# Optimization experiments

Hardware: AMD Instinct MI355X
Metric: run time of the kernel (lower is better)

The kernel has to match this reference:

```python
import jax, jax.numpy as jnp
import numpy as np

N_NODES = 50000
N_EDGES = 1600000
NFEAT, NHID, NCLASS = 512, 128, 40


def setup_inputs() -> dict:
    key = jax.random.key(0)
    ks = jax.random.split(key, 10)
    x = jax.random.normal(ks[0], (N_NODES, NFEAT), dtype=jnp.float32)
    edge_src = jax.random.randint(ks[1], (N_EDGES,), 0, N_NODES, dtype=jnp.int32)
    edge_dst = jax.random.randint(ks[2], (N_EDGES,), 0, N_NODES, dtype=jnp.int32)
    edge_weight = jax.random.uniform(ks[3], (N_EDGES,), dtype=jnp.float32)
    # GraphConvolution params: gc1 (nfeat->nhid), one additional (nhid->nhid), gc2 (nhid->nclass)
    s1 = 1.0 / np.sqrt(NHID)
    s2 = 1.0 / np.sqrt(NCLASS)
    W1 = jax.random.uniform(ks[4], (NFEAT, NHID), minval=-s1, maxval=s1, dtype=jnp.float32)
    b1 = jax.random.uniform(ks[5], (NHID,), minval=-s1, maxval=s1, dtype=jnp.float32)
    Wh = jax.random.uniform(ks[6], (NHID, NHID), minval=-s1, maxval=s1, dtype=jnp.float32)
    bh = jax.random.uniform(ks[7], (NHID,), minval=-s1, maxval=s1, dtype=jnp.float32)
    W2 = jax.random.uniform(ks[8], (NHID, NCLASS), minval=-s2, maxval=s2, dtype=jnp.float32)
    b2 = jax.random.uniform(ks[9], (NCLASS,), minval=-s2, maxval=s2, dtype=jnp.float32)
    return {"x": x, "edge_src": edge_src, "edge_dst": edge_dst, "edge_weight": edge_weight,
            "W1": W1, "b1": b1, "Wh": Wh, "bh": bh, "W2": W2, "b2": b2}


def reference(x, edge_src, edge_dst, edge_weight, W1, b1, Wh, bh, W2, b2):
    def spmm(h):
        # out[i] = sum_j adj[i, j] * h[j]  with adj given as weighted edge list (src=j, dst=i)
        return jax.ops.segment_sum(edge_weight[:, None] * h[edge_src], edge_dst,
                                   num_segments=x.shape[0])

    def gconv(h, W, b):
        return spmm(h @ W) + b  # dense transform then sparse aggregation

    h = jax.nn.relu(gconv(x, W1, b1))       # gc1
    h = jax.nn.relu(gconv(h, Wh, bh))        # additional hidden layer
    h = gconv(h, W2, b2)                     # gc2
    return jax.nn.log_softmax(h, axis=1)
```

## Files before the change

kernel.cpp:

```cpp
#include <hip/hip_runtime.h>
#include <hip/hip_bf16.h>
#include <math.h>

#define N_NODES 50000
#define N_EDGES 1600000
#define NFEAT 512
#define NHID 128
#define NCLASS 40

#define NBUCKETS 196
#define BUCKET_CAP 16384

typedef __attribute__((ext_vector_type(8))) short bf16x8;
typedef __attribute__((ext_vector_type(4))) float f32x4;

static __device__ __forceinline__ float asfloat_u32(unsigned int u) {
    union { unsigned int u; float f; } c;
    c.u = u;
    return c.f;
}
static __device__ __forceinline__ unsigned int asu32_f(float f) {
    union { float f; unsigned int u; } c;
    c.f = f;
    return c.u;
}
static __device__ __forceinline__ unsigned short f2bf(float f) {
    union { float f; unsigned int u; } c;
    c.f = f;
    unsigned int r = c.u + 0x7FFFu + ((c.u >> 16) & 1u);
    return (unsigned short)(r >> 16);
}

__global__ __launch_bounds__(256) void prep_kernel(const float* __restrict__ W1,
                                                   unsigned short* __restrict__ Wt1,
                                                   const float* __restrict__ Wh,
                                                   unsigned short* __restrict__ Wth,
                                                   int* __restrict__ bucketCursor) {
    int idx = blockIdx.x * 256 + threadIdx.x;
    if (idx < NFEAT * NHID) {
        int k = idx >> 7;
        int n = idx & 127;
        Wt1[(size_t)n * NFEAT + k] = f2bf(W1[idx]);
    } else if (idx < NFEAT * NHID + NHID * NHID) {
        int j = idx - NFEAT * NHID;
        int k = j >> 7;
        int n = j & 127;
        Wth[(size_t)n * NHID + k] = f2bf(Wh[j]);
    } else {
        int j = idx - (NFEAT * NHID + NHID * NHID);
        if (j < NBUCKETS) bucketCursor[j] = j * BUCKET_CAP;
    }
}

#define LDP 40
#define GEMM_LDS_BYTES ((64 + 128) * LDP * 2)

template <bool A_IS_BF16>
static __device__ __forceinline__ void gemm64_body(const void* __restrict__ Ap,
                                                   const unsigned short* __restrict__ Wt,
                                                   unsigned short* __restrict__ C,
                                                   const int M, const int K,
                                                   char* smem, int bid) {
    unsigned short* As = (unsigned short*)smem;
    unsigned short* Bs = (unsigned short*)smem + 64 * LDP;
    const int tid = threadIdx.x;
    const int wave = tid >> 6;
    const int lane = tid & 63;
    const int ln = lane & 15;
    const int quad = lane >> 4;
    const int row0 = bid * 64;

    const int ar = tid >> 2;
    const int ac = (tid & 3) * 8;
    const bool arOk = (row0 + ar) < M;
    const int bn = tid >> 1;
    const int bk = (tid & 1) * 16;

    f32x4 acc[8];
#pragma unroll
    for (int t = 0; t < 8; ++t) acc[t] = (f32x4){0.f, 0.f, 0.f, 0.f};

    for (int kc = 0; kc < K; kc += 32) {
        bf16x8 va;
        if (A_IS_BF16) {
            if (arOk) {
                va = *(const bf16x8*)((const unsigned short*)Ap +
                                      (size_t)(row0 + ar) * K + kc + ac);
            } else {
#pragma unroll
                for (int i = 0; i < 8; ++i) va[i] = 0;
            }
        } else {
            if (arOk) {
                const float* Af = (const float*)Ap + (size_t)(row0 + ar) * K + kc + ac;
                float4 f0 = *(const float4*)(Af);
                float4 f1 = *(const float4*)(Af + 4);
                va[0] = (short)f2bf(f0.x); va[1] = (short)f2bf(f0.y);
                va[2] = (short)f2bf(f0.z); va[3] = (short)f2bf(f0.w);
                va[4] = (short)f2bf(f1.x); va[5] = (short)f2bf(f1.y);
                va[6] = (short)f2bf(f1.z); va[7] = (short)f2bf(f1.w);
            } else {
#pragma unroll
                for (int i = 0; i < 8; ++i) va[i] = 0;
            }
        }
        const unsigned short* Bg = Wt + (size_t)bn * K + kc + bk;
        bf16x8 vb0 = *(const bf16x8*)Bg;
        bf16x8 vb1 = *(const bf16x8*)(Bg + 8);

        __syncthreads();
        *(bf16x8*)&As[ar * LDP + ac] = va;
        *(bf16x8*)&Bs[bn * LDP + bk] = vb0;
        *(bf16x8*)&Bs[bn * LDP + bk + 8] = vb1;
        __syncthreads();

        bf16x8 a = *(const bf16x8*)&As[(wave * 16 + ln) * LDP + quad * 8];
#pragma unroll
        for (int t = 0; t < 8; ++t) {
            bf16x8 b = *(const bf16x8*)&Bs[(t * 16 + ln) * LDP + quad * 8];
            acc[t] = __builtin_amdgcn_mfma_f32_16x16x32_bf16(a, b, acc[t], 0, 0, 0);
        }
    }

#pragma unroll
    for (int t = 0; t < 8; ++t) {
#pragma unroll
        for (int r = 0; r < 4; ++r) {
            int row = row0 + wave * 16 + quad * 4 + r;
            if (row < M) C[(size_t)row * 128 + t * 16 + ln] = f2bf(acc[t][r]);
        }
    }
}

static __device__ __forceinline__ void bin_body(const int* __restrict__ src,
                                                const int* __restrict__ dst,
                                                const float* __restrict__ w,
                                                int* __restrict__ bucketCursor,
                                                uint2* __restrict__ binned,
                                                int n, char* smem, int bid) {
    int* hist = (int*)smem;
    int* cur = (int*)smem + NBUCKETS;
    const int tid = threadIdx.x;
    const int base = bid * 4096;
    if (tid < NBUCKETS) hist[tid] = 0;
    __syncthreads();
#pragma unroll
    for (int r = 0; r < 16; ++r) {
        int e = base + r * 256 + tid;
        if (e < n) atomicAdd(&hist[dst[e] >> 8], 1);
    }
    __syncthreads();
    if (tid < NBUCKETS && hist[tid] > 0)
        cur[tid] = atomicAdd(&bucketCursor[tid], hist[tid]);
    __syncthreads();
#pragma unroll
    for (int r = 0; r < 16; ++r) {
        int e = base + r * 256 + tid;
        if (e < n) {
            int d = dst[e];
            int pos = atomicAdd(&cur[d >> 8], 1);
            uint2 rec;
            rec.x = (unsigned int)src[e] | ((unsigned int)(d & 255) << 16);
            rec.y = asu32_f(w[e]);
            binned[pos] = rec;
        }
    }
}

#define GEMM1_BLOCKS 782
#define BIN_BLOCKS 391
__global__ __launch_bounds__(256) void fused_gemm1_bin(const float* __restrict__ x,
                                                       const unsigned short* __restrict__ Wt1,
                                                       unsigned short* __restrict__ tb,
                                                       const int* __restrict__ src,
                                                       const int* __restrict__ dst,
                                                       const float* __restrict__ w,
                                                       int* __restrict__ bucketCursor,
                                                       uint2* __restrict__ binned) {
    __shared__ char smem[GEMM_LDS_BYTES];
    if (blockIdx.x < GEMM1_BLOCKS) {
        gemm64_body<false>(x, Wt1, tb, N_NODES, NFEAT, smem, blockIdx.x);
    } else {
        bin_body(src, dst, w, bucketCursor, binned, N_EDGES, smem,
                 blockIdx.x - GEMM1_BLOCKS);
    }
}

__global__ __launch_bounds__(256) void gemm64_l2(const unsigned short* __restrict__ A,
                                                 const unsigned short* __restrict__ Wt,
                                                 unsigned short* __restrict__ C) {
    __shared__ char smem[GEMM_LDS_BYTES];
    gemm64_body<true>(A, Wt, C, N_NODES, NHID, smem, blockIdx.x);
}

__global__ __launch_bounds__(256) void build_csr(const uint2* __restrict__ binned,
                                                 const int* __restrict__ bucketCursor,
                                                 unsigned int* __restrict__ pairs,
                                                 int* __restrict__ row_ptr) {
    __shared__ int bs[256];
    __shared__ int hist[256];
    __shared__ int sc[256];
    __shared__ int cur[256];
    const int b = blockIdx.x;
    const int tid = threadIdx.x;

    int c = (tid < NBUCKETS) ? (bucketCursor[tid] - tid * BUCKET_CAP) : 0;
    bs[tid] = c;
    __syncthreads();
    for (int off = 1; off < 256; off <<= 1) {
        int t = (tid >= off) ? bs[tid - off] : 0;
        __syncthreads();
        bs[tid] += t;
        __syncthreads();
    }
    const int cnt = bucketCursor[b] - b * BUCKET_CAP;
    const int segStart = bs[b] - cnt;
    if (b == NBUCKETS - 1 && tid == 0) row_ptr[N_NODES] = bs[NBUCKETS - 1];
    const uint2* seg = binned + (size_t)b * BUCKET_CAP;

    hist[tid] = 0;
    __syncthreads();
    for (int i = tid; i < cnt; i += 256)
        atomicAdd(&hist[seg[i].x >> 16], 1);
    __syncthreads();
    int v = hist[tid];
    sc[tid] = v;
    __syncthreads();
    for (int off = 1; off < 256; off <<= 1) {
        int t = (tid >= off) ? sc[tid - off] : 0;
        __syncthreads();
        sc[tid] += t;
        __syncthreads();
    }
    int excl = sc[tid] - v;
    int node = b * 256 + tid;
    if (node < N_NODES) row_ptr[node] = segStart + excl;
    cur[tid] = segStart + excl;
    __syncthreads();
    for (int i = tid; i < cnt; i += 256) {
        uint2 p = seg[i];
        int pos = atomicAdd(&cur[p.x >> 16], 1);
        pairs[pos] = (p.x & 0xFFFFu) | ((unsigned int)f2bf(asfloat_u32(p.y)) << 16);
    }
}

__global__ __launch_bounds__(256) void gemm_n40_bf16A(const unsigned short* __restrict__ A,
                                                      const float* __restrict__ Bm,
                                                      unsigned short* __restrict__ C, int M) {
    __shared__ float As[64][132];
    __shared__ float Bs[128 * 40];
    const int tid = threadIdx.x;
    const int tr = tid >> 2;
    const int tc = tid & 3;
    const int row0 = blockIdx.x * 64;

#pragma unroll
    for (int q = tid; q < 2048; q += 256) {
        int r = q >> 5;
        int c = (q & 31) << 2;
        int row = row0 + r;
        uint2 u = make_uint2(0u, 0u);
        if (row < M) u = *(const uint2*)(A + (size_t)row * 128 + c);
        As[r][c + 0] = asfloat_u32(u.x << 16);
        As[r][c + 1] = asfloat_u32(u.x & 0xFFFF0000u);
        As[r][c + 2] = asfloat_u32(u.y << 16);
        As[r][c + 3] = asfloat_u32(u.y & 0xFFFF0000u);
    }
    for (int q = tid; q < 128 * 40; q += 256) Bs[q] = Bm[q];
    __syncthreads();

    float acc[10];
#pragma unroll
    for (int j = 0; j < 10; ++j) acc[j] = 0.f;

    for (int k = 0; k < 128; ++k) {
        float a = As[tr][k];
#pragma unroll
        for (int j = 0; j < 10; ++j) acc[j] += a * Bs[k * 40 + tc * 10 + j];
    }

    int row = row0 + tr;
    if (row < M) {
#pragma unroll
        for (int j = 0; j < 10; ++j) C[(size_t)row * 40 + tc * 10 + j] = f2bf(acc[j]);
    }
}

__global__ __launch_bounds__(256) void spmm_bias_relu_bf16(const unsigned short* __restrict__ t,
                                                           const int* __restrict__ row_ptr,
                                                           const unsigned int* __restrict__ pairs,
                                                           const float* __restrict__ bias,
                                                           unsigned short* __restrict__ out) {
    const int node = blockIdx.x * 4 + (threadIdx.x >> 6);
    const int lane = threadIdx.x & 63;
    const int e0 = row_ptr[node];
    const int e1 = row_ptr[node + 1];
    float ax = 0.f, ay = 0.f;
    int e = e0;
    for (; e + 8 <= e1; e += 8) {
        unsigned int p0 = pairs[e],     p1 = pairs[e + 1], p2 = pairs[e + 2], p3 = pairs[e + 3];
        unsigned int p4 = pairs[e + 4], p5 = pairs[e + 5], p6 = pairs[e + 6], p7 = pairs[e + 7];
        unsigned int v0 = *(const unsigned int*)(t + (size_t)(p0 & 0xFFFFu) * 128 + lane * 2);
        unsigned int v1 = *(const unsigned int*)(t + (size_t)(p1 & 0xFFFFu) * 128 + lane * 2);
        unsigned int v2 = *(const unsigned int*)(t + (size_t)(p2 & 0xFFFFu) * 128 + lane * 2);
        unsigned int v3 = *(const unsigned int*)(t + (size_t)(p3 & 0xFFFFu) * 128 + lane * 2);
        unsigned int v4 = *(const unsigned int*)(t + (size_t)(p4 & 0xFFFFu) * 128 + lane * 2);
        unsigned int v5 = *(const unsigned int*)(t + (size_t)(p5 & 0xFFFFu) * 128 + lane * 2);
        unsigned int v6 = *(const unsigned int*)(t + (size_t)(p6 & 0xFFFFu) * 128 + lane * 2);
        unsigned int v7 = *(const unsigned int*)(t + (size_t)(p7 & 0xFFFFu) * 128 + lane * 2);
        float w0 = asfloat_u32(p0 & 0xFFFF0000u), w1 = asfloat_u32(p1 & 0xFFFF0000u);
        float w2 = asfloat_u32(p2 & 0xFFFF0000u), w3 = asfloat_u32(p3 & 0xFFFF0000u);
        float w4 = asfloat_u32(p4 & 0xFFFF0000u), w5 = asfloat_u32(p5 & 0xFFFF0000u);
        float w6 = asfloat_u32(p6 & 0xFFFF0000u), w7 = asfloat_u32(p7 & 0xFFFF0000u);
        ax += w0 * asfloat_u32(v0 << 16); ay += w0 * asfloat_u32(v0 & 0xFFFF0000u);
        ax += w1 * asfloat_u32(v1 << 16); ay += w1 * asfloat_u32(v1 & 0xFFFF0000u);
        ax += w2 * asfloat_u32(v2 << 16); ay += w2 * asfloat_u32(v2 & 0xFFFF0000u);
        ax += w3 * asfloat_u32(v3 << 16); ay += w3 * asfloat_u32(v3 & 0xFFFF0000u);
        ax += w4 * asfloat_u32(v4 << 16); ay += w4 * asfloat_u32(v4 & 0xFFFF0000u);
        ax += w5 * asfloat_u32(v5 << 16); ay += w5 * asfloat_u32(v5 & 0xFFFF0000u);
        ax += w6 * asfloat_u32(v6 << 16); ay += w6 * asfloat_u32(v6 & 0xFFFF0000u);
        ax += w7 * asfloat_u32(v7 << 16); ay += w7 * asfloat_u32(v7 & 0xFFFF0000u);
    }
    for (; e < e1; ++e) {
        unsigned int p = pairs[e];
        float w = asfloat_u32(p & 0xFFFF0000u);
        unsigned int v = *(const unsigned int*)(t + (size_t)(p & 0xFFFFu) * 128 + lane * 2);
        ax += w * asfloat_u32(v << 16);
        ay += w * asfloat_u32(v & 0xFFFF0000u);
    }
    float2 b = *(const float2*)&bias[lane * 2];
    ax = fmaxf(ax + b.x, 0.f);
    ay = fmaxf(ay + b.y, 0.f);
    unsigned int packed = ((unsigned int)f2bf(ax)) | (((unsigned int)f2bf(ay)) << 16);
    *(unsigned int*)(out + (size_t)node * 128 + lane * 2) = packed;
}

__global__ __launch_bounds__(256) void spmm_logsoftmax(const unsigned short* __restrict__ t,
                                                       const int* __restrict__ row_ptr,
                                                       const unsigned int* __restrict__ pairs,
                                                       const float* __restrict__ bias,
                                                       float* __restrict__ out) {
    const int node = blockIdx.x * 4 + (threadIdx.x >> 6);
    const int lane = threadIdx.x & 63;
    const int e0 = row_ptr[node];
    const int e1 = row_ptr[node + 1];
    const bool act = lane < NCLASS;
    float acc = 0.f;
    int e = e0;
    for (; e + 4 <= e1; e += 4) {
        unsigned int p0 = pairs[e], p1 = pairs[e + 1], p2 = pairs[e + 2], p3 = pairs[e + 3];
        if (act) {
            float v0 = asfloat_u32((unsigned int)t[(size_t)(p0 & 0xFFFFu) * NCLASS + lane] << 16);
            float v1 = asfloat_u32((unsigned int)t[(size_t)(p1 & 0xFFFFu) * NCLASS + lane] << 16);
            float v2 = asfloat_u32((unsigned int)t[(size_t)(p2 & 0xFFFFu) * NCLASS + lane] << 16);
            float v3 = asfloat_u32((unsigned int)t[(size_t)(p3 & 0xFFFFu) * NCLASS + lane] << 16);
            acc += asfloat_u32(p0 & 0xFFFF0000u) * v0 + asfloat_u32(p1 & 0xFFFF0000u) * v1 +
                   asfloat_u32(p2 & 0xFFFF0000u) * v2 + asfloat_u32(p3 & 0xFFFF0000u) * v3;
        }
    }
    for (; e < e1; ++e) {
        unsigned int p = pairs[e];
        if (act)
            acc += asfloat_u32(p & 0xFFFF0000u) *
                   asfloat_u32((unsigned int)t[(size_t)(p & 0xFFFFu) * NCLASS + lane] << 16);
    }
    float logit = act ? (acc + bias[lane]) : -INFINITY;
    float m = logit;
#pragma unroll
    for (int off = 32; off; off >>= 1) m = fmaxf(m, __shfl_xor(m, off));
    float ex = act ? __expf(logit - m) : 0.f;
    float ssum = ex;
#pragma unroll
    for (int off = 32; off; off >>= 1) ssum += __shfl_xor(ssum, off);
    if (act) out[(size_t)node * NCLASS + lane] = logit - m - __logf(ssum);
}


extern "C" void kernel_launch(void* const* d_in, const int* in_sizes, int n_in,
                              void* d_out, int out_size, void* d_ws, size_t ws_size,
                              hipStream_t stream) {
    const float* x = (const float*)d_in[0];
    const int* edge_src = (const int*)d_in[1];
    const int* edge_dst = (const int*)d_in[2];
    const float* edge_weight = (const float*)d_in[3];
    const float* W1 = (const float*)d_in[4];
    const float* b1 = (const float*)d_in[5];
    const float* Wh = (const float*)d_in[6];
    const float* bh = (const float*)d_in[7];
    const float* W2 = (const float*)d_in[8];
    const float* b2 = (const float*)d_in[9];
    float* out = (float*)d_out;

    size_t off = 0;
    auto carve = [&](size_t bytes) {
        void* p = (char*)d_ws + off;
        off += (bytes + 511) & ~(size_t)511;
        return p;
    };
    unsigned short* tb = (unsigned short*)carve((size_t)N_NODES * 128 * 2);
    unsigned short* hb = (unsigned short*)carve((size_t)N_NODES * 128 * 2);
    unsigned short* t3 = (unsigned short*)carve((size_t)N_NODES * NCLASS * 2);
    unsigned short* Wt1 = (unsigned short*)carve((size_t)NFEAT * NHID * 2);
    unsigned short* Wth = (unsigned short*)carve((size_t)NHID * NHID * 2);
    int* row_ptr = (int*)carve((size_t)(N_NODES + 4) * 4);
    int* bucketCursor = (int*)carve((size_t)NBUCKETS * 4);
    uint2* binned = (uint2*)carve((size_t)NBUCKETS * BUCKET_CAP * 8);
    unsigned int* pairs = (unsigned int*)carve((size_t)N_EDGES * 4);
    (void)ws_size; (void)n_in; (void)in_sizes; (void)out_size;

    const int prepBlocks = (NFEAT * NHID + NHID * NHID + NBUCKETS + 255) / 256;
    const int spmmBlocks = N_NODES / 4;
    const int gemmBlocks = (N_NODES + 63) / 64;

    prep_kernel<<<prepBlocks, 256, 0, stream>>>(W1, Wt1, Wh, Wth, bucketCursor);

    fused_gemm1_bin<<<GEMM1_BLOCKS + BIN_BLOCKS, 256, 0, stream>>>(
        x, Wt1, tb, edge_src, edge_dst, edge_weight, bucketCursor, binned);

    build_csr<<<NBUCKETS, 256, 0, stream>>>(binned, bucketCursor, pairs, row_ptr);

    spmm_bias_relu_bf16<<<spmmBlocks, 256, 0, stream>>>(tb, row_ptr, pairs, b1, hb);

    gemm64_l2<<<gemmBlocks, 256, 0, stream>>>(hb, Wth, tb);
    spmm_bias_relu_bf16<<<spmmBlocks, 256, 0, stream>>>(tb, row_ptr, pairs, bh, hb);

    gemm_n40_bf16A<<<gemmBlocks, 256, 0, stream>>>(hb, W2, t3, N_NODES);
    spmm_logsoftmax<<<spmmBlocks, 256, 0, stream>>>(t3, row_ptr, pairs, b2, out);
}
```

Before: 437.1 us.

## Use MFMA for layer-3 GEMM, widen CSR build, split SpMM edges across half-waves

Replaces the scalar FP32 128x40 GEMM with a bf16 MFMA kernel that uses a transposed, zero-padded W2 (48 columns) prepared in the prep kernel. The CSR build moves to 1024-thread blocks so each bucket's histogram and scatter passes have more parallelism. The hidden-layer SpMM now has the two half-waves take alternate edges with 4 features per lane, then combines them with a shuffle. The log-softmax SpMM unroll goes from 4 to 8. Together these aim to cut FLOP cost and raise memory-level parallelism in the gathers, at the cost of extra shuffles and padded MFMA work.

```diff
diff --git a/kernel.cpp b/kernel.cpp
--- a/kernel.cpp
+++ b/kernel.cpp
@@ -35,6 +35,8 @@
                                                    unsigned short* __restrict__ Wt1,
                                                    const float* __restrict__ Wh,
                                                    unsigned short* __restrict__ Wth,
+                                                   const float* __restrict__ W2,
+                                                   unsigned short* __restrict__ Wt2,
                                                    int* __restrict__ bucketCursor) {
     int idx = blockIdx.x * 256 + threadIdx.x;
     if (idx < NFEAT * NHID) {
@@ -46,8 +48,13 @@
         int k = j >> 7;
         int n = j & 127;
         Wth[(size_t)n * NHID + k] = f2bf(Wh[j]);
+    } else if (idx < NFEAT * NHID + NHID * NHID + 64 * NHID) {
+        int j = idx - (NFEAT * NHID + NHID * NHID);
+        int n = j & 63;
+        int k = j >> 6;
+        Wt2[(size_t)n * NHID + k] = (n < NCLASS) ? f2bf(W2[(size_t)k * NCLASS + n]) : 0;
     } else {
-        int j = idx - (NFEAT * NHID + NHID * NHID);
+        int j = idx - (NFEAT * NHID + NHID * NHID + 64 * NHID);
         if (j < NBUCKETS) bucketCursor[j] = j * BUCKET_CAP;
     }
 }
@@ -193,10 +200,10 @@
     gemm64_body<true>(A, Wt, C, N_NODES, NHID, smem, blockIdx.x);
 }
 
-__global__ __launch_bounds__(256) void build_csr(const uint2* __restrict__ binned,
-                                                 const int* __restrict__ bucketCursor,
-                                                 unsigned int* __restrict__ pairs,
-                                                 int* __restrict__ row_ptr) {
+__global__ __launch_bounds__(1024) void build_csr(const uint2* __restrict__ binned,
+                                                  const int* __restrict__ bucketCursor,
+                                                  unsigned int* __restrict__ pairs,
+                                                  int* __restrict__ row_ptr) {
     __shared__ int bs[256];
     __shared__ int hist[256];
     __shared__ int sc[256];
@@ -204,13 +211,14 @@
     const int b = blockIdx.x;
     const int tid = threadIdx.x;
 
-    int c = (tid < NBUCKETS) ? (bucketCursor[tid] - tid * BUCKET_CAP) : 0;
-    bs[tid] = c;
+    if (tid < 256) bs[tid] = (tid < NBUCKETS) ? (bucketCursor[tid] - tid * BUCKET_CAP) : 0;
+    if (tid < 256) hist[tid] = 0;
     __syncthreads();
     for (int off = 1; off < 256; off <<= 1) {
-        int t = (tid >= off) ? bs[tid - off] : 0;
-        __syncthreads();
-        bs[tid] += t;
+        int t = 0;
+        if (tid < 256 && tid >= off) t = bs[tid - off];
+        __syncthreads();
+        if (tid < 256) bs[tid] += t;
         __syncthreads();
     }
     const int cnt = bucketCursor[b] - b * BUCKET_CAP;
@@ -218,71 +226,95 @@
     if (b == NBUCKETS - 1 && tid == 0) row_ptr[N_NODES] = bs[NBUCKETS - 1];
     const uint2* seg = binned + (size_t)b * BUCKET_CAP;
 
-    hist[tid] = 0;
-    __syncthreads();
-    for (int i = tid; i < cnt; i += 256)
+    for (int i = tid; i < cnt; i += 1024)
         atomicAdd(&hist[seg[i].x >> 16], 1);
     __syncthreads();
-    int v = hist[tid];
-    sc[tid] = v;
+    if (tid < 256) {
+        int v = hist[tid];
+        sc[tid] = v;
+    }
     __syncthreads();
     for (int off = 1; off < 256; off <<= 1) {
-        int t = (tid >= off) ? sc[tid - off] : 0;
-        __syncthreads();
-        sc[tid] += t;
-        __syncthreads();
-    }
-    int excl = sc[tid] - v;
-    int node = b * 256 + tid;
-    if (node < N_NODES) row_ptr[node] = segStart + excl;
-    cur[tid] = segStart + excl;
-    __syncthreads();
-    for (int i = tid; i < cnt; i += 256) {
+        int t = 0;
+        if (tid < 256 && tid >= off) t = sc[tid - off];
+        __syncthreads();
+        if (tid < 256) sc[tid] += t;
+        __syncthreads();
+    }
+    if (tid < 256) {
+        int excl = sc[tid] - hist[tid];
+        int node = b * 256 + tid;
+        if (node < N_NODES) row_ptr[node] = segStart + excl;
+        cur[tid] = segStart + excl;
+    }
+    __syncthreads();
+    for (int i = tid; i < cnt; i += 1024) {
         uint2 p = seg[i];
         int pos = atomicAdd(&cur[p.x >> 16], 1);
         pairs[pos] = (p.x & 0xFFFFu) | ((unsigned int)f2bf(asfloat_u32(p.y)) << 16);
     }
 }
 
-__global__ __launch_bounds__(256) void gemm_n40_bf16A(const unsigned short* __restrict__ A,
-                                                      const float* __restrict__ Bm,
-                                                      unsigned short* __restrict__ C, int M) {
-    __shared__ float As[64][132];
-    __shared__ float Bs[128 * 40];
+#define LDP2 136
+__global__ __launch_bounds__(256) void gemm_n48(const unsigned short* __restrict__ A,
+                                                const unsigned short* __restrict__ Wt2,
+                                                unsigned short* __restrict__ C, int M) {
+    __shared__ unsigned short As[64 * LDP2];
+    __shared__ unsigned short Bs[48 * LDP2];
     const int tid = threadIdx.x;
-    const int tr = tid >> 2;
-    const int tc = tid & 3;
+    const int wave = tid >> 6;
+    const int lane = tid & 63;
+    const int ln = lane & 15;
+    const int quad = lane >> 4;
     const int row0 = blockIdx.x * 64;
 
 #pragma unroll
-    for (int q = tid; q < 2048; q += 256) {
-        int r = q >> 5;
-        int c = (q & 31) << 2;
-        int row = row0 + r;
-        uint2 u = make_uint2(0u, 0u);
-        if (row < M) u = *(const uint2*)(A + (size_t)row * 128 + c);
-        As[r][c + 0] = asfloat_u32(u.x << 16);
-        As[r][c + 1] = asfloat_u32(u.x & 0xFFFF0000u);
-        As[r][c + 2] = asfloat_u32(u.y << 16);
-        As[r][c + 3] = asfloat_u32(u.y & 0xFFFF0000u);
-    }
-    for (int q = tid; q < 128 * 40; q += 256) Bs[q] = Bm[q];
-    __syncthreads();
-
-    float acc[10];
-#pragma unroll
-    for (int j = 0; j < 10; ++j) acc[j] = 0.f;
-
-    for (int k = 0; k < 128; ++k) {
-        float a = As[tr][k];
-#pragma unroll
-        for (int j = 0; j < 10; ++j) acc[j] += a * Bs[k * 40 + tc * 10 + j];
-    }
-
-    int row = row0 + tr;
-    if (row < M) {
-#pragma unroll
-        for (int j = 0; j < 10; ++j) C[(size_t)row * 40 + tc * 10 + j] = f2bf(acc[j]);
+    for (int i = 0; i < 4; ++i) {
+        int q = tid + 256 * i;
+        int r = q >> 4;
+        int c = (q & 15) * 8;
+        bf16x8 v;
+        if (row0 + r < M) {
+            v = *(const bf16x8*)(A + (size_t)(row0 + r) * 128 + c);
+        } else {
+#pragma unroll
+            for (int j = 0; j < 8; ++j) v[j] = 0;
+        }
+        *(bf16x8*)&As[r * LDP2 + c] = v;
+    }
+#pragma unroll
+    for (int i = 0; i < 3; ++i) {
+        int q = tid + 256 * i;
+        int r = q >> 4;
+        int c = (q & 15) * 8;
+        *(bf16x8*)&Bs[r * LDP2 + c] = *(const bf16x8*)(Wt2 + (size_t)r * 128 + c);
+    }
+    __syncthreads();
+
+    f32x4 acc[3];
+#pragma unroll
+    for (int t = 0; t < 3; ++t) acc[t] = (f32x4){0.f, 0.f, 0.f, 0.f};
+
+#pragma unroll
+    for (int kc = 0; kc < 128; kc += 32) {
+        bf16x8 a = *(const bf16x8*)&As[(wave * 16 + ln) * LDP2 + kc + quad * 8];
+#pragma unroll
+        for (int t = 0; t < 3; ++t) {
+            bf16x8 b = *(const bf16x8*)&Bs[(t * 16 + ln) * LDP2 + kc + quad * 8];
+            acc[t] = __builtin_amdgcn_mfma_f32_16x16x32_bf16(a, b, acc[t], 0, 0, 0);
+        }
+    }
+
+#pragma unroll
+    for (int t = 0; t < 3; ++t) {
+        int col = t * 16 + ln;
+        if (col < NCLASS) {
+#pragma unroll
+            for (int r = 0; r < 4; ++r) {
+                int row = row0 + wave * 16 + quad * 4 + r;
+                if (row < M) C[(size_t)row * NCLASS + col] = f2bf(acc[t][r]);
+            }
+        }
     }
 }
 
@@ -293,46 +325,62 @@
                                                            unsigned short* __restrict__ out) {
     const int node = blockIdx.x * 4 + (threadIdx.x >> 6);
     const int lane = threadIdx.x & 63;
+    const int half = lane >> 5;
+    const int fq = (lane & 31) * 4;
     const int e0 = row_ptr[node];
     const int e1 = row_ptr[node + 1];
-    float ax = 0.f, ay = 0.f;
+    float a0 = 0.f, a1 = 0.f, a2 = 0.f, a3 = 0.f;
     int e = e0;
-    for (; e + 8 <= e1; e += 8) {
-        unsigned int p0 = pairs[e],     p1 = pairs[e + 1], p2 = pairs[e + 2], p3 = pairs[e + 3];
-        unsigned int p4 = pairs[e + 4], p5 = pairs[e + 5], p6 = pairs[e + 6], p7 = pairs[e + 7];
-        unsigned int v0 = *(const unsigned int*)(t + (size_t)(p0 & 0xFFFFu) * 128 + lane * 2);
-        unsigned int v1 = *(const unsigned int*)(t + (size_t)(p1 & 0xFFFFu) * 128 + lane * 2);
-        unsigned int v2 = *(const unsigned int*)(t + (size_t)(p2 & 0xFFFFu) * 128 + lane * 2);
-        unsigned int v3 = *(const unsigned int*)(t + (size_t)(p3 & 0xFFFFu) * 128 + lane * 2);
-        unsigned int v4 = *(const unsigned int*)(t + (size_t)(p4 & 0xFFFFu) * 128 + lane * 2);
-        unsigned int v5 = *(const unsigned int*)(t + (size_t)(p5 & 0xFFFFu) * 128 + lane * 2);
-        unsigned int v6 = *(const unsigned int*)(t + (size_t)(p6 & 0xFFFFu) * 128 + lane * 2);
-        unsigned int v7 = *(const unsigned int*)(t + (size_t)(p7 & 0xFFFFu) * 128 + lane * 2);
-        float w0 = asfloat_u32(p0 & 0xFFFF0000u), w1 = asfloat_u32(p1 & 0xFFFF0000u);
-        float w2 = asfloat_u32(p2 & 0xFFFF0000u), w3 = asfloat_u32(p3 & 0xFFFF0000u);
-        float w4 = asfloat_u32(p4 & 0xFFFF0000u), w5 = asfloat_u32(p5 & 0xFFFF0000u);
-        float w6 = asfloat_u32(p6 & 0xFFFF0000u), w7 = asfloat_u32(p7 & 0xFFFF0000u);
-        ax += w0 * asfloat_u32(v0 << 16); ay += w0 * asfloat_u32(v0 & 0xFFFF0000u);
-        ax += w1 * asfloat_u32(v1 << 16); ay += w1 * asfloat_u32(v1 & 0xFFFF0000u);
-        ax += w2 * asfloat_u32(v2 << 16); ay += w2 * asfloat_u32(v2 & 0xFFFF0000u);
-        ax += w3 * asfloat_u32(v3 << 16); ay += w3 * asfloat_u32(v3 & 0xFFFF0000u);
-        ax += w4 * asfloat_u32(v4 << 16); ay += w4 * asfloat_u32(v4 & 0xFFFF0000u);
-        ax += w5 * asfloat_u32(v5 << 16); ay += w5 * asfloat_u32(v5 & 0xFFFF0000u);
-        ax += w6 * asfloat_u32(v6 << 16); ay += w6 * asfloat_u32(v6 & 0xFFFF0000u);
-        ax += w7 * asfloat_u32(v7 << 16); ay += w7 * asfloat_u32(v7 & 0xFFFF0000u);
-    }
-    for (; e < e1; ++e) {
+    for (; e + 16 <= e1; e += 16) {
+        unsigned int p[8];
+        uint2 v[8];
+#pragma unroll
+        for (int i = 0; i < 8; ++i) p[i] = pairs[e + 2 * i + half];
+#pragma unroll
+        for (int i = 0; i < 8; ++i)
+            v[i] = *(const uint2*)(t + (size_t)(p[i] & 0xFFFFu) * 128 + fq);
+#pragma unroll
+        for (int i = 0; i < 8; ++i) {
+            float w = asfloat_u32(p[i] & 0xFFFF0000u);
+            a0 += w * asfloat_u32(v[i].x << 16);
+            a1 += w * asfloat_u32(v[i].x & 0xFFFF0000u);
+            a2 += w * asfloat_u32(v[i].y << 16);
+            a3 += w * asfloat_u32(v[i].y & 0xFFFF0000u);
+        }
+    }
+    for (; e + 2 <= e1; e += 2) {
+        unsigned int p = pairs[e + half];
+        uint2 v = *(const uint2*)(t + (size_t)(p & 0xFFFFu) * 128 + fq);
+        float w = asfloat_u32(p & 0xFFFF0000u);
+        a0 += w * asfloat_u32(v.x << 16);
+        a1 += w * asfloat_u32(v.x & 0xFFFF0000u);
+        a2 += w * asfloat_u32(v.y << 16);
+        a3 += w * asfloat_u32(v.y & 0xFFFF0000u);
+    }
+    if (e < e1 && half == 0) {
         unsigned int p = pairs[e];
+        uint2 v = *(const uint2*)(t + (size_t)(p & 0xFFFFu) * 128 + fq);
         float w = asfloat_u32(p & 0xFFFF0000u);
-        unsigned int v = *(const unsigned int*)(t + (size_t)(p & 0xFFFFu) * 128 + lane * 2);
-        ax += w * asfloat_u32(v << 16);
-        ay += w * asfloat_u32(v & 0xFFFF0000u);
-    }
-    float2 b = *(const float2*)&bias[lane * 2];
-    ax = fmaxf(ax + b.x, 0.f);
-    ay = fmaxf(ay + b.y, 0.f);
-    unsigned int packed = ((unsigned int)f2bf(ax)) | (((unsigned int)f2bf(ay)) << 16);
-    *(unsigned int*)(out + (size_t)node * 128 + lane * 2) = packed;
+        a0 += w * asfloat_u32(v.x << 16);
+        a1 += w * asfloat_u32(v.x & 0xFFFF0000u);
+        a2 += w * asfloat_u32(v.y << 16);
+        a3 += w * asfloat_u32(v.y & 0xFFFF0000u);
+    }
+    a0 += __shfl_xor(a0, 32);
+    a1 += __shfl_xor(a1, 32);
+    a2 += __shfl_xor(a2, 32);
+    a3 += __shfl_xor(a3, 32);
+    if (half == 0) {
+        float4 b = *(const float4*)&bias[fq];
+        a0 = fmaxf(a0 + b.x, 0.f);
+        a1 = fmaxf(a1 + b.y, 0.f);
+        a2 = fmaxf(a2 + b.z, 0.f);
+        a3 = fmaxf(a3 + b.w, 0.f);
+        uint2 o;
+        o.x = ((unsigned int)f2bf(a0)) | (((unsigned int)f2bf(a1)) << 16);
+        o.y = ((unsigned int)f2bf(a2)) | (((unsigned int)f2bf(a3)) << 16);
+        *(uint2*)(out + (size_t)node * 128 + fq) = o;
+    }
 }
 
 __global__ __launch_bounds__(256) void spmm_logsoftmax(const unsigned short* __restrict__ t,
@@ -347,15 +395,17 @@
     const bool act = lane < NCLASS;
     float acc = 0.f;
     int e = e0;
-    for (; e + 4 <= e1; e += 4) {
-        unsigned int p0 = pairs[e], p1 = pairs[e + 1], p2 = pairs[e + 2], p3 = pairs[e + 3];
+    for (; e + 8 <= e1; e += 8) {
+        unsigned int p[8];
+#pragma unroll
+        for (int i = 0; i < 8; ++i) p[i] = pairs[e + i];
         if (act) {
-            float v0 = asfloat_u32((unsigned int)t[(size_t)(p0 & 0xFFFFu) * NCLASS + lane] << 16);
-            float v1 = asfloat_u32((unsigned int)t[(size_t)(p1 & 0xFFFFu) * NCLASS + lane] << 16);
-            float v2 = asfloat_u32((unsigned int)t[(size_t)(p2 & 0xFFFFu) * NCLASS + lane] << 16);
-            float v3 = asfloat_u32((unsigned int)t[(size_t)(p3 & 0xFFFFu) * NCLASS + lane] << 16);
-            acc += asfloat_u32(p0 & 0xFFFF0000u) * v0 + asfloat_u32(p1 & 0xFFFF0000u) * v1 +
-                   asfloat_u32(p2 & 0xFFFF0000u) * v2 + asfloat_u32(p3 & 0xFFFF0000u) * v3;
+            float v[8];
+#pragma unroll
+            for (int i = 0; i < 8; ++i)
+                v[i] = asfloat_u32((unsigned int)t[(size_t)(p[i] & 0xFFFFu) * NCLASS + lane] << 16);
+#pragma unroll
+            for (int i = 0; i < 8; ++i) acc += asfloat_u32(p[i] & 0xFFFF0000u) * v[i];
         }
     }
     for (; e < e1; ++e) {
@@ -402,28 +452,30 @@
     unsigned short* t3 = (unsigned short*)carve((size_t)N_NODES * NCLASS * 2);
     unsigned short* Wt1 = (unsigned short*)carve((size_t)NFEAT * NHID * 2);
     unsigned short* Wth = (unsigned short*)carve((size_t)NHID * NHID * 2);
+    unsigned short* Wt2 = (unsigned short*)carve((size_t)64 * NHID * 2);
     int* row_ptr = (int*)carve((size_t)(N_NODES + 4) * 4);
     int* bucketCursor = (int*)carve((size_t)NBUCKETS * 4);
     uint2* binned = (uint2*)carve((size_t)NBUCKETS * BUCKET_CAP * 8);
     unsigned int* pairs = (unsigned int*)carve((size_t)N_EDGES * 4);
     (void)ws_size; (void)n_in; (void)in_sizes; (void)out_size;
 
-    const int prepBlocks = (NFEAT * NHID + NHID * NHID + NBUCKETS + 255) / 256;
+    const int prepBlocks =
+        (NFEAT * NHID + NHID * NHID + 64 * NHID + NBUCKETS + 255) / 256;
     const int spmmBlocks = N_NODES / 4;
     const int gemmBlocks = (N_NODES + 63) / 64;
 
-    prep_kernel<<<prepBlocks, 256, 0, stream>>>(W1, Wt1, Wh, Wth, bucketCursor);
+    prep_kernel<<<prepBlocks, 256, 0, stream>>>(W1, Wt1, Wh, Wth, W2, Wt2, bucketCursor);
 
     fused_gemm1_bin<<<GEMM1_BLOCKS + BIN_BLOCKS, 256, 0, stream>>>(
         x, Wt1, tb, edge_src, edge_dst, edge_weight, bucketCursor, binned);
 
-    build_csr<<<NBUCKETS, 256, 0, stream>>>(binned, bucketCursor, pairs, row_ptr);
+    build_csr<<<NBUCKETS, 1024, 0, stream>>>(binned, bucketCursor, pairs, row_ptr);
 
     spmm_bias_relu_bf16<<<spmmBlocks, 256, 0, stream>>>(tb, row_ptr, pairs, b1, hb);
 
     gemm64_l2<<<gemmBlocks, 256, 0, stream>>>(hb, Wth, tb);
     spmm_bias_relu_bf16<<<spmmBlocks, 256, 0, stream>>>(tb, row_ptr, pairs, bh, hb);
 
-    gemm_n40_bf16A<<<gemmBlocks, 256, 0, stream>>>(hb, W2, t3, N_NODES);
+    gemm_n48<<<gemmBlocks, 256, 0, stream>>>(hb, Wt2, t3, N_NODES);
     spmm_logsoftmax<<<spmmBlocks, 256, 0, stream>>>(t3, row_ptr, pairs, b2, out);
 }
```

New measurement: 396.5 us. 1.1x faster.
